# Kernel tuning notes

Measured on AMD Instinct MI355X. Metric: run time of the kernel, lower is better.

The kernel has to match this reference:

```python
import jax, jax.numpy as jnp
import numpy as np
from jax import lax

E = 16          # num_experts
CAP = 256       # capacity
MAX_IT = 3      # max_iterations
LPF = 2.0       # load_penalty_factor
DTEMP = 2.0     # diversity_temp
MIN_USAGE = 0.05
NC = 10         # num_classes
TC = 256        # trunk_channels
B = 2048
MIN_TOK = max(1, int(B * MIN_USAGE))        # 102
K_STATIC = min(B, max(CAP, MIN_TOK))        # static top-k width per expert claim


def setup_inputs() -> dict:
    key = jax.random.key(0)
    ks = jax.random.split(key, 16)
    d = {}
    d['x'] = jax.random.normal(ks[0], (B, 3, 32, 32), jnp.float32)
    chans = [(3, 32), (32, 64), (64, 128), (128, 256)]
    for i, (ci, co) in enumerate(chans, 1):
        d[f'cw{i}'] = jax.random.normal(ks[i], (co, ci, 3, 3), jnp.float32) * (1.0 / np.sqrt(ci * 9))
        d[f'cb{i}'] = jnp.zeros((co,), jnp.float32)
        d[f'g{i}'] = jnp.ones((co,), jnp.float32)
        d[f'be{i}'] = jnp.zeros((co,), jnp.float32)
        d[f'm{i}'] = jnp.zeros((co,), jnp.float32)
        d[f'v{i}'] = jnp.ones((co,), jnp.float32)
    d['gw1'] = jax.random.normal(ks[5], (E, TC, TC // 2), jnp.float32) * 0.05
    d['gb1'] = jnp.zeros((E, TC // 2), jnp.float32)
    d['gw2'] = jax.random.normal(ks[6], (E, TC // 2), jnp.float32) * 0.05
    d['gb2'] = jnp.zeros((E,), jnp.float32)
    d['cls_w'] = jax.random.normal(ks[7], (E, NC, TC), jnp.float32) * 0.01
    d['cls_b'] = jnp.zeros((E, NC), jnp.float32)
    d['usage_ema'] = jnp.ones((E,), jnp.float32) / E
    return d


def _conv_bn_relu(x, w, b, g, beta, m, v):
    y = lax.conv_general_dilated(x, w, (1, 1), 'SAME', dimension_numbers=('NCHW', 'OIHW', 'NCHW'))
    y = y + b[None, :, None, None]
    scale = (g / jnp.sqrt(v + 1e-5))[None, :, None, None]
    return jax.nn.relu((y - m[None, :, None, None]) * scale + beta[None, :, None, None])


def _maxpool2(x):
    return lax.reduce_window(x, -jnp.inf, lax.max, (1, 1, 2, 2), (1, 1, 2, 2), 'VALID')


def _forward(x, cw1, cb1, g1, be1, m1, v1, cw2, cb2, g2, be2, m2, v2,
             cw3, cb3, g3, be3, m3, v3, cw4, cb4, g4, be4, m4, v4,
             gw1, gb1, gw2, gb2, cls_w, cls_b, usage_ema):
    # trunk (eval-mode BN)
    h = _conv_bn_relu(x, cw1, cb1, g1, be1, m1, v1)
    h = _conv_bn_relu(h, cw2, cb2, g2, be2, m2, v2)
    h = _maxpool2(h)
    h = _conv_bn_relu(h, cw3, cb3, g3, be3, m3, v3)
    h = _conv_bn_relu(h, cw4, cb4, g4, be4, m4, v4)
    h = _maxpool2(h)
    feats = h.mean(axis=(2, 3))  # AdaptiveAvgPool2d(1)+Flatten -> [B, TC]

    # per-expert classifier heads
    logits_e = jnp.einsum('bd,ecd->bec', feats, cls_w) + cls_b[None]  # [B,E,NC]
    probs = jax.nn.softmax(logits_e, axis=2)
    ent = -(probs * jnp.log(jnp.clip(probs, 1e-12))).sum(axis=2)      # [B,E]
    confidence = -ent

    # per-expert gates (vectorized over experts); dropout is identity in eval
    hidden = jax.nn.relu(jnp.einsum('bd,edh->beh', feats, gw1) + gb1[None])
    expert_scores = (jnp.einsum('beh,eh->be', hidden, gw2) + gb2[None]) / DTEMP

    routing_scores = 0.6 * expert_scores + 0.4 * confidence - LPF * usage_ema[None]

    # iterative capacity-constrained routing (eval: expert order 0..E-1)
    D = jnp.zeros((B, E), bool)
    loads = jnp.zeros((E,), jnp.float32)
    avail = jnp.ones((B,), bool)
    ranks = jnp.arange(K_STATIC)
    for it in range(MAX_IT):
        # penalty from loads at the START of the iteration
        pscores = routing_scores - (it + 1) * LPF * loads[None]
        for j in range(E):
            sj = jnp.where(avail, pscores[:, j], -jnp.inf)
            vc = avail.sum().astype(jnp.int32)
            rc = jnp.maximum(0, CAP - loads[j].astype(jnp.int32))
            ntc = jnp.where((rc == 0) | (vc == 0), 0,
                            jnp.maximum(jnp.minimum(rc, vc), jnp.minimum(MIN_TOK, vc)))
            _, idx = lax.top_k(sj, K_STATIC)
            take = ranks < ntc
            claimed = jnp.zeros((B,), bool).at[idx].set(take)
            D = D.at[:, j].set(D[:, j] | claimed)
            avail = avail & ~claimed
            loads = loads.at[j].add(ntc.astype(jnp.float32))

    # fallback: sequentially assign leftover tokens to least-loaded of top-3
    def fb(carry, inp):
        Dc, lc = carry
        sc, av, i = inp
        _, t3 = lax.top_k(sc, 3)
        best = t3[jnp.argmin(lc[t3])]
        Dc = Dc.at[i, best].set(Dc[i, best] | av)
        lc = lc.at[best].add(av.astype(jnp.float32))
        return (Dc, lc), None

    (D, loads), _ = lax.scan(fb, (D, loads), (routing_scores, avail, jnp.arange(B)))

    Df = D.astype(jnp.float32)
    active = routing_scores * Df
    active = active - active.max(axis=1, keepdims=True)
    weights = jax.nn.softmax(active + (Df - 1.0) * 1e9, axis=1)
    final_logits = (weights[:, :, None] * logits_e).sum(axis=1)
    return final_logits, routing_scores, D


def reference(x, cw1, cb1, g1, be1, m1, v1, cw2, cb2, g2, be2, m2, v2,
              cw3, cb3, g3, be3, m3, v3, cw4, cb4, g4, be4, m4, v4,
              gw1, gb1, gw2, gb2, cls_w, cls_b, usage_ema):
    return _forward(x, cw1, cb1, g1, be1, m1, v1, cw2, cb2, g2, be2, m2, v2,
                    cw3, cb3, g3, be3, m3, v3, cw4, cb4, g4, be4, m4, v4,
                    gw1, gb1, gw2, gb2, cls_w, cls_b, usage_ema)
```

## Files before the change

kernel.cpp:

```cpp
#include <hip/hip_runtime.h>

typedef __attribute__((ext_vector_type(8))) short short8;
typedef __attribute__((ext_vector_type(4))) float f32x4;

__device__ __forceinline__ unsigned short f2bf(float f) {
  unsigned u = __float_as_uint(f);
  unsigned r = (u + 0x7fffu + ((u >> 16) & 1u)) >> 16;
  return (unsigned short)r;
}
__device__ __forceinline__ float bf2f(unsigned short h) {
  return __uint_as_float(((unsigned)h) << 16);
}

__global__ __launch_bounds__(256) void bnprep_kernel(
    const float* __restrict__ g, const float* __restrict__ be,
    const float* __restrict__ m, const float* __restrict__ v,
    const float* __restrict__ b, float* __restrict__ A, float* __restrict__ C, int n)
{
  int i = blockIdx.x * 256 + threadIdx.x;
  if (i < n) {
    float s = g[i] / sqrtf(v[i] + 1e-5f);
    A[i] = s;
    C[i] = (b[i] - m[i]) * s + be[i];
  }
}

__global__ __launch_bounds__(256) void wprep2_kernel(
    const float* __restrict__ w, unsigned short* __restrict__ wPk, int CO, int CI)
{
  int NCB = CI / 32, NF = CO / 16;
  int total = 9 * NCB * NF * 64;
  int idx = blockIdx.x * 256 + threadIdx.x;
  if (idx >= total) return;
  int lane = idx & 63;
  int unit = idx >> 6;
  int f = unit % NF;
  int cb = (unit / NF) % NCB;
  int s = unit / (NF * NCB);
  int co = f * 16 + (lane & 15);
  int ci0 = cb * 32 + (lane >> 4) * 8;
  long base = (long)unit * 1024 + lane * 8;
  #pragma unroll
  for (int j = 0; j < 8; ++j) {
    float v = w[((long)co * CI + ci0 + j) * 9 + s];
    unsigned short h = f2bf(v);
    unsigned short l = f2bf(v - bf2f(h));
    wPk[base + j] = h;
    wPk[base + 512 + j] = l;
  }
}

__global__ __launch_bounds__(512, 2) void conv12_kernel(
    const float* __restrict__ xin, const float* __restrict__ cw1,
    const float* __restrict__ A1p, const float* __restrict__ C1p,
    const unsigned short* __restrict__ wPk, const float* __restrict__ Ap,
    const float* __restrict__ Cp, unsigned short* __restrict__ outA)
{
  constexpr int TY = 16, TX = 32;
  constexpr int PXW = TX + 2;
  constexpr int PXT = (TY + 2) * PXW;
  constexpr int PLSTR = PXT * 8 + 8;
  constexpr int NF = 4;
  __shared__ alignas(16) unsigned short smem[8 * PLSTR];
  __shared__ alignas(16) float sx[2160];
  __shared__ alignas(16) float sw[864];

  const int nwg = gridDim.x;
  const int orig = blockIdx.x;
  const int q = nwg >> 3, r = nwg & 7;
  const int xcd = orig & 7, pos = orig >> 3;
  const int bx = (xcd < r ? xcd * (q + 1) : r * (q + 1) + (xcd - r) * q) + pos;

  const int img = bx >> 1;
  const int tY0 = (bx & 1) * 16;

  const int tid = threadIdx.x;
  const int lane = tid & 63;
  const int lx = lane & 15, kg = lane >> 4;
  const int w = tid >> 6;

  for (int i = tid; i < 2160; i += 512) {
    int c = i / 720, rem = i - c * 720;
    int yy = rem / 36, xx2 = rem - yy * 36;
    int gy = tY0 + yy - 2, gx = xx2 - 2;
    sx[i] = (gy >= 0 && gy < 32 && gx >= 0 && gx < 32)
            ? xin[(long)img * 3072 + c * 1024 + gy * 32 + gx] : 0.f;
  }
  for (int i = tid; i < 864; i += 512) {
    int co = i & 31, kk = i >> 5;
    sw[kk * 32 + co] = cw1[(long)co * 27 + kk];
  }
  __syncthreads();

  #pragma unroll 1
  for (int p = 0; p < 2; ++p) {
    int px = p * 512 + tid;
    if (px < PXT) {
      int ry = px / PXW, rx = px - ry * PXW;
      int gy = tY0 + ry - 1, gx = rx - 1;
      if (gy >= 0 && gy < 32 && gx >= 0 && gx < 32) {
        #pragma unroll 1
        for (int half = 0; half < 2; ++half) {
          float acc[16];
          #pragma unroll
          for (int j = 0; j < 16; ++j) acc[j] = 0.f;
          #pragma unroll
          for (int c = 0; c < 3; ++c) {
            #pragma unroll
            for (int k = 0; k < 9; ++k) {
              int dy = k / 3, dx = k - 3 * (k / 3);
              float iv = sx[c * 720 + (ry + dy) * 36 + rx + dx];
              const float4* w4 = (const float4*)(sw + (c * 9 + k) * 32 + half * 16);
              #pragma unroll
              for (int q2 = 0; q2 < 4; ++q2) {
                float4 wv = w4[q2];
                acc[4 * q2 + 0] += iv * wv.x; acc[4 * q2 + 1] += iv * wv.y;
                acc[4 * q2 + 2] += iv * wv.z; acc[4 * q2 + 3] += iv * wv.w;
              }
            }
          }
          #pragma unroll
          for (int j2 = 0; j2 < 2; ++j2) {
            short8 hv, lv;
            #pragma unroll
            for (int j = 0; j < 8; ++j) {
              int co = half * 16 + j2 * 8 + j;
              float vv = fmaxf(acc[j2 * 8 + j] * A1p[co] + C1p[co], 0.f);
              unsigned short h = f2bf(vv);
              hv[j] = (short)h;
              lv[j] = (short)f2bf(vv - bf2f(h));
            }
            int plane = half * 2 + j2;
            *(short8*)(smem + plane * PLSTR + px * 8) = hv;
            *(short8*)(smem + (plane + 4) * PLSTR + px * 8) = lv;
          }
        }
      } else {
        short8 zz = {0, 0, 0, 0, 0, 0, 0, 0};
        #pragma unroll
        for (int cc = 0; cc < 8; ++cc)
          *(short8*)(smem + cc * PLSTR + px * 8) = zz;
      }
    }
  }
  __syncthreads();

  f32x4 acc[4][4];
  #pragma unroll
  for (int i = 0; i < 4; ++i)
    #pragma unroll
    for (int j = 0; j < 4; ++j) acc[i][j] = (f32x4){0.f, 0.f, 0.f, 0.f};

  for (int s = 0; s < 9; ++s) {
    const int ky = s / 3, kx = s - 3 * (s / 3);
    const long ub = ((long)(s * NF)) * 1024 + lane * 8;
    short8 bh[4], bl[4];
    #pragma unroll
    for (int nf = 0; nf < 4; ++nf) {
      bh[nf] = *(const short8*)(wPk + ub + nf * 1024);
      bl[nf] = *(const short8*)(wPk + ub + nf * 1024 + 512);
    }
    #pragma unroll
    for (int mf = 0; mf < 4; ++mf) {
      const int yoff = mf >> 1;
      const int xb = (mf & 1) * 16;
      const int y = w * 2 + yoff;
      const int pxa = (y + ky) * PXW + xb + kx + lx;
      short8 ah = *(const short8*)(smem + kg * PLSTR + pxa * 8);
      short8 al = *(const short8*)(smem + (kg + 4) * PLSTR + pxa * 8);
      #pragma unroll
      for (int nf = 0; nf < 4; ++nf)
        acc[mf][nf] = __builtin_amdgcn_mfma_f32_16x16x32_bf16(ah, bh[nf], acc[mf][nf], 0, 0, 0);
      #pragma unroll
      for (int nf = 0; nf < 4; ++nf)
        acc[mf][nf] = __builtin_amdgcn_mfma_f32_16x16x32_bf16(ah, bl[nf], acc[mf][nf], 0, 0, 0);
      #pragma unroll
      for (int nf = 0; nf < 4; ++nf)
        acc[mf][nf] = __builtin_amdgcn_mfma_f32_16x16x32_bf16(al, bh[nf], acc[mf][nf], 0, 0, 0);
    }
  }
  __syncthreads();

  float Ar[4], Cr[4];
  #pragma unroll
  for (int nf = 0; nf < 4; ++nf) {
    int co = nf * 16 + lx;
    Ar[nf] = Ap[co]; Cr[nf] = Cp[co];
  }

  unsigned short* slice = smem + w * 2048;
  const int py = (tY0 >> 1) + w;
  #pragma unroll
  for (int xf = 0; xf < 2; ++xf) {
    #pragma unroll
    for (int rp = 0; rp < 2; ++rp) {
      int ox = xf * 8 + 2 * kg + rp;
      #pragma unroll
      for (int nf = 0; nf < 4; ++nf) {
        float v0 = fmaxf(fmaxf(acc[xf][nf][2 * rp], acc[xf][nf][2 * rp + 1]),
                         fmaxf(acc[xf + 2][nf][2 * rp], acc[xf + 2][nf][2 * rp + 1]));
        float vv = fmaxf(v0 * Ar[nf] + Cr[nf], 0.f);
        unsigned short h = f2bf(vv);
        unsigned short l = f2bf(vv - bf2f(h));
        slice[(ox * 2 + 0) * 64 + nf * 16 + lx] = h;
        slice[(ox * 2 + 1) * 64 + nf * 16 + lx] = l;
      }
    }
  }
  #pragma unroll
  for (int v = 0; v < 4; ++v) {
    int hoff = lane * 8 + v * 512;
    int x2 = hoff >> 7, rem = hoff & 127;
    int seg = rem >> 6, inner = rem & 63;
    short8 d = *(const short8*)(slice + hoff);
    *(short8*)(outA + ((long)img * 256 + py * 16 + x2) * 128 + seg * 64 + inner) = d;
  }
}

template<int H, int CI, int CO, int COB, int TY, int TX, int MODE>
__global__ __launch_bounds__(512, 2) void convmf4_kernel(
    const unsigned short* __restrict__ actIn, const unsigned short* __restrict__ wPk,
    const float* __restrict__ Ap, const float* __restrict__ Cp,
    void* __restrict__ outP)
{
  constexpr int NCB = CI / 32;
  constexpr int NF  = CO / 16;
  constexpr int NCOG = COB / 64;
  constexpr int NPXG = 8 / NCOG;
  constexpr int ROWS_PG = TY / NPXG;
  constexpr int FRX = TX / 16;
  constexpr int PXW = TX + 2;
  constexpr int PXT = (TY + 2) * PXW;
  constexpr int PLSTR = PXT * 8 + 8;
  constexpr int TILES_Y = H / TY;
  constexpr int CBLK = CO / COB;
  constexpr int TPI = TILES_Y * CBLK;
  constexpr int PIX_IN = 2 * CI;
  __shared__ alignas(16) unsigned short smem[8 * PLSTR];

  const int nwg = gridDim.x;
  const int orig = blockIdx.x;
  const int q = nwg >> 3, r = nwg & 7;
  const int xcd = orig & 7, pos = orig >> 3;
  const int bx = (xcd < r ? xcd * (q + 1) : r * (q + 1) + (xcd - r) * q) + pos;

  const int img = bx / TPI;
  const int sub = bx % TPI;
  const int tY0 = (sub % TILES_Y) * TY;
  const int blkco = sub / TILES_Y;

  const int tid = threadIdx.x;
  const int lane = tid & 63;
  const int lx = lane & 15, kg = lane >> 4;
  const int w = tid >> 6;
  const int pxg = w % NPXG, cog = w / NPXG;

  f32x4 acc[4][4];
  #pragma unroll
  for (int i = 0; i < 4; ++i)
    #pragma unroll
    for (int j = 0; j < 4; ++j) acc[i][j] = (f32x4){0.f, 0.f, 0.f, 0.f};

  for (int cb = 0; cb < NCB; ++cb) {
    if (cb) __syncthreads();
    for (int t2 = tid; t2 < PXT * 8; t2 += 512) {
      int px = t2 >> 3, c = t2 & 7;
      int ry = px / PXW, rx = px - ry * PXW;
      int gy = tY0 + ry - 1, gx = rx - 1;
      float4 v = (float4){0.f, 0.f, 0.f, 0.f};
      if (gy >= 0 && gy < H && gx >= 0 && gx < H) {
        int coff = (c < 4) ? (cb * 32 + c * 8) : (CI + cb * 32 + (c - 4) * 8);
        v = *(const float4*)(actIn + ((long)img * H * H + gy * H + gx) * PIX_IN + coff);
      }
      *(float4*)(smem + c * PLSTR + px * 8) = v;
    }
    __syncthreads();

    for (int s = 0; s < 9; ++s) {
      const int ky = s / 3, kx = s - 3 * (s / 3);
      const long ub = ((long)(s * NCB + cb) * NF + blkco * (COB / 16) + cog * 4) * 1024
                      + lane * 8;
      short8 bh[4], bl[4];
      #pragma unroll
      for (int nf = 0; nf < 4; ++nf) {
        bh[nf] = *(const short8*)(wPk + ub + nf * 1024);
        bl[nf] = *(const short8*)(wPk + ub + nf * 1024 + 512);
      }
      #pragma unroll
      for (int mf = 0; mf < 4; ++mf) {
        const int yoff = (FRX == 2) ? (mf >> 1) : mf;
        const int xb = (FRX == 2) ? ((mf & 1) * 16) : 0;
        const int y = pxg * ROWS_PG + yoff;
        const int pxa = (y + ky) * PXW + xb + kx + lx;
        short8 ah = *(const short8*)(smem + kg * PLSTR + pxa * 8);
        short8 al = *(const short8*)(smem + (kg + 4) * PLSTR + pxa * 8);
        #pragma unroll
        for (int nf = 0; nf < 4; ++nf)
          acc[mf][nf] = __builtin_amdgcn_mfma_f32_16x16x32_bf16(ah, bh[nf], acc[mf][nf], 0, 0, 0);
        #pragma unroll
        for (int nf = 0; nf < 4; ++nf)
          acc[mf][nf] = __builtin_amdgcn_mfma_f32_16x16x32_bf16(ah, bl[nf], acc[mf][nf], 0, 0, 0);
        #pragma unroll
        for (int nf = 0; nf < 4; ++nf)
          acc[mf][nf] = __builtin_amdgcn_mfma_f32_16x16x32_bf16(al, bh[nf], acc[mf][nf], 0, 0, 0);
      }
    }
  }
  __syncthreads();

  float Ar[4], Cr[4];
  #pragma unroll
  for (int nf = 0; nf < 4; ++nf) {
    int co = blkco * COB + cog * 64 + nf * 16 + lx;
    Ar[nf] = Ap[co]; Cr[nf] = Cp[co];
  }

  if (MODE == 0) {
    unsigned short* outA = (unsigned short*)outP;
    unsigned short* slice = smem + w * 2048;
    #pragma unroll
    for (int mf = 0; mf < 4; ++mf) {
      int y = tY0 + pxg * ROWS_PG + mf;
      #pragma unroll
      for (int rr = 0; rr < 4; ++rr) {
        int x = 4 * kg + rr;
        #pragma unroll
        for (int nf = 0; nf < 4; ++nf) {
          float vv = fmaxf(acc[mf][nf][rr] * Ar[nf] + Cr[nf], 0.f);
          unsigned short h = f2bf(vv);
          unsigned short l = f2bf(vv - bf2f(h));
          slice[(x * 2 + 0) * 64 + nf * 16 + lx] = h;
          slice[(x * 2 + 1) * 64 + nf * 16 + lx] = l;
        }
      }
      #pragma unroll
      for (int v = 0; v < 4; ++v) {
        int hoff = lane * 8 + v * 512;
        int x2 = hoff >> 7, rem = hoff & 127;
        int seg = rem >> 6, inner = rem & 63;
        short8 d = *(const short8*)(slice + hoff);
        *(short8*)(outA + ((long)img * 256 + y * 16 + x2) * (2 * CO)
                   + seg * CO + blkco * COB + cog * 64 + inner) = d;
      }
    }
  } else {
    float psum[4] = {0.f, 0.f, 0.f, 0.f};
    #pragma unroll
    for (int nf = 0; nf < 4; ++nf) {
      #pragma unroll
      for (int mfp = 0; mfp < 2; ++mfp) {
        #pragma unroll
        for (int rp = 0; rp < 2; ++rp) {
          float v = fmaxf(fmaxf(acc[2 * mfp][nf][2 * rp], acc[2 * mfp][nf][2 * rp + 1]),
                          fmaxf(acc[2 * mfp + 1][nf][2 * rp], acc[2 * mfp + 1][nf][2 * rp + 1]));
          psum[nf] += fmaxf(v * Ar[nf] + Cr[nf], 0.f);
        }
      }
    }
    #pragma unroll
    for (int nf = 0; nf < 4; ++nf) {
      psum[nf] += __shfl_xor(psum[nf], 16);
      psum[nf] += __shfl_xor(psum[nf], 32);
    }
    __syncthreads();
    float* sR = (float*)smem;
    if (kg == 0) {
      #pragma unroll
      for (int nf = 0; nf < 4; ++nf) sR[w * 64 + nf * 16 + lx] = psum[nf];
    }
    __syncthreads();
    if (tid < COB) {
      int ct = tid >> 6, ci_ = tid & 63;
      float s = 0.f;
      #pragma unroll
      for (int p = 0; p < NPXG; ++p) s += sR[(ct * NPXG + p) * 64 + ci_];
      ((float*)outP)[(long)img * 256 + blkco * COB + tid] = s * (1.f / 64.f);
    }
  }
}

__global__ __launch_bounds__(256) void heads2_kernel(
    const float* __restrict__ feats, const float* __restrict__ gw1,
    const float* __restrict__ gb1, const float* __restrict__ gw2,
    const float* __restrict__ gb2, const float* __restrict__ clsw,
    const float* __restrict__ clsb, const float* __restrict__ usage,
    float* __restrict__ logits_e, float* __restrict__ rs_out)
{
  __shared__ float sF[64 * 257];
  __shared__ float sLg[4 * 64 * 10];
  __shared__ float sRed[4 * 64];
  const int tid = threadIdx.x;
  const int b0 = blockIdx.x * 64;
  const int e  = blockIdx.y;

  for (int idx = tid; idx < 64 * 64; idx += 256) {
    int t = idx >> 6, dg = idx & 63;
    float4 v = ((const float4*)(feats + (long)(b0 + t) * 256))[dg];
    float* p = sF + t * 257 + dg * 4;
    p[0] = v.x; p[1] = v.y; p[2] = v.z; p[3] = v.w;
  }
  __syncthreads();

  const int t  = tid & 63;
  const int hw = __builtin_amdgcn_readfirstlane(tid >> 6);

  {
    float acc[10];
    #pragma unroll
    for (int c = 0; c < 10; ++c) acc[c] = 0.f;
    const float* fp = sF + t * 257 + hw * 64;
    const float* cw = clsw + (long)e * 2560 + hw * 64;
    for (int dd = 0; dd < 64; ++dd) {
      float f = fp[dd];
      #pragma unroll
      for (int c = 0; c < 10; ++c) acc[c] += f * cw[c * 256 + dd];
    }
    #pragma unroll
    for (int c = 0; c < 10; ++c) sLg[(hw * 64 + t) * 10 + c] = acc[c];
  }
  {
    float gacc[32];
    #pragma unroll
    for (int j = 0; j < 32; ++j) gacc[j] = 0.f;
    const float* wb = gw1 + ((long)e * 256) * 128 + hw * 32;
    const float* fp = sF + t * 257;
    for (int d = 0; d < 256; ++d) {
      float f = fp[d];
      const float4* w4 = (const float4*)(wb + (long)d * 128);
      #pragma unroll
      for (int qq = 0; qq < 8; ++qq) {
        float4 wv = w4[qq];
        gacc[4 * qq + 0] += f * wv.x; gacc[4 * qq + 1] += f * wv.y;
        gacc[4 * qq + 2] += f * wv.z; gacc[4 * qq + 3] += f * wv.w;
      }
    }
    float s = 0.f;
    const float* b1 = gb1 + e * 128 + hw * 32;
    const float* w2 = gw2 + e * 128 + hw * 32;
    #pragma unroll
    for (int j = 0; j < 32; ++j) s += fmaxf(gacc[j] + b1[j], 0.f) * w2[j];
    sRed[hw * 64 + t] = s;
  }
  __syncthreads();

  if (tid < 64) {
    float es = (sRed[t] + sRed[64 + t] + sRed[128 + t] + sRed[192 + t] + gb2[e]) * 0.5f;
    float lg[10];
    #pragma unroll
    for (int c = 0; c < 10; ++c)
      lg[c] = sLg[t * 10 + c] + sLg[(64 + t) * 10 + c]
            + sLg[(128 + t) * 10 + c] + sLg[(192 + t) * 10 + c] + clsb[e * 10 + c];
    float mx = lg[0];
    #pragma unroll
    for (int c = 1; c < 10; ++c) mx = fmaxf(mx, lg[c]);
    float S = 0.f, ps[10];
    #pragma unroll
    for (int c = 0; c < 10; ++c) { ps[c] = expf(lg[c] - mx); S += ps[c]; }
    float inv = 1.f / S, ent = 0.f;
    #pragma unroll
    for (int c = 0; c < 10; ++c) { float p = ps[c] * inv; ent -= p * logf(fmaxf(p, 1e-12f)); }
    float rsv = 0.6f * es + 0.4f * (-ent) - 2.0f * usage[e];
    rs_out[(long)(b0 + t) * 16 + e] = rsv;
    #pragma unroll
    for (int c = 0; c < 10; ++c)
      logits_e[((long)(b0 + t) * 16 + e) * 10 + c] = lg[c];
  }
}

__global__ __launch_bounds__(1024) void sort_kernel(
    const float* __restrict__ rs, unsigned* __restrict__ sortedIdx)
{
  __shared__ unsigned long long sk[2048];
  const int e = blockIdx.x;
  const unsigned tid = threadIdx.x;
  for (int i = tid; i < 2048; i += 1024) {
    float f = rs[(long)i * 16 + e];
    unsigned u = __float_as_uint(f);
    u ^= (u >> 31) ? 0xFFFFFFFFu : 0x80000000u;
    sk[i] = ((unsigned long long)(~u) << 32) | (unsigned)i;
  }
  for (unsigned k = 2; k <= 2048; k <<= 1) {
    for (unsigned j = k >> 1; j > 0; j >>= 1) {
      __syncthreads();
      unsigned i = ((tid & ~(j - 1)) << 1) | (tid & (j - 1));
      unsigned p = i | j;
      bool asc = ((i & k) == 0);
      unsigned long long a = sk[i], b = sk[p];
      if ((a > b) == asc) { sk[i] = b; sk[p] = a; }
    }
  }
  __syncthreads();
  for (int i = tid; i < 2048; i += 1024)
    sortedIdx[(long)e * 2048 + i] = (unsigned)(sk[i] & 0xFFFFFFFFull);
}

__global__ __launch_bounds__(1024) void routing_kernel(
    const unsigned* __restrict__ sortedIdx, const float* __restrict__ rs,
    float* __restrict__ Dout, unsigned* __restrict__ dmaskOut)
{
  __shared__ unsigned char sAvail[2048];
  __shared__ unsigned sDm[2048];
  __shared__ int sLoads[16];
  __shared__ int sWaveCnt[16];
  __shared__ int sNtc, sVC;
  const int tid = threadIdx.x;
  const int lane = tid & 63, wave = tid >> 6;
  for (int i = tid; i < 2048; i += 1024) { sAvail[i] = 1; sDm[i] = 0; }
  if (tid < 16) sLoads[tid] = 0;
  if (tid == 0) sVC = 2048;
  __syncthreads();
  for (int it = 0; it < 3; ++it) {
    for (int j = 0; j < 16; ++j) {
      if (tid == 0) {
        int rc = 256 - sLoads[j]; if (rc < 0) rc = 0;
        int vc = sVC, ntc = 0;
        if (rc > 0 && vc > 0) {
          int a = rc < vc ? rc : vc;
          int b2 = vc < 102 ? vc : 102;
          ntc = a > b2 ? a : b2;
        }
        sNtc = ntc; sLoads[j] += ntc; sVC -= ntc;
      }
      __syncthreads();
      const int ntc = sNtc;
      if (ntc > 0) {
        int base = 0;
        for (int p = 0; p < 2; ++p) {
          int i = p * 1024 + tid;
          unsigned tok = sortedIdx[(long)j * 2048 + i];
          int fl = sAvail[tok] ? 1 : 0;
          unsigned long long bm = __ballot(fl);
          if (lane == 0) sWaveCnt[wave] = __popcll(bm);
          __syncthreads();
          int off = base;
          for (int w = 0; w < wave; ++w) off += sWaveCnt[w];
          int pre = off + __popcll(bm & ((1ull << lane) - 1ull));
          if (fl && pre < ntc) { sAvail[tok] = 0; sDm[tok] |= (1u << j); }
          int tot = base;
          for (int w = 0; w < 16; ++w) tot += sWaveCnt[w];
          base = tot;
          __syncthreads();
        }
      }
      __syncthreads();
    }
  }
  if (tid == 0 && sVC > 0) {
    for (int i = 0; i < 2048; ++i) {
      if (!sAvail[i]) continue;
      float s0 = -3.4e38f, s1 = s0, s2 = s0; int e0 = 0, e1 = 0, e2 = 0;
      for (int e = 0; e < 16; ++e) {
        float s = rs[i * 16 + e];
        if (s > s0)      { s2 = s1; e2 = e1; s1 = s0; e1 = e0; s0 = s; e0 = e; }
        else if (s > s1) { s2 = s1; e2 = e1; s1 = s;  e1 = e; }
        else if (s > s2) { s2 = s;  e2 = e; }
      }
      int best = e0, bl = sLoads[e0];
      if (sLoads[e1] < bl) { best = e1; bl = sLoads[e1]; }
      if (sLoads[e2] < bl) { best = e2; bl = sLoads[e2]; }
      sDm[i] |= (1u << best);
      sLoads[best] += 1;
    }
  }
  __syncthreads();
  for (int idx = tid; idx < 2048 * 16; idx += 1024) {
    int tok = idx >> 4, e = idx & 15;
    Dout[idx] = ((sDm[tok] >> e) & 1u) ? 1.0f : 0.0f;
  }
  for (int i = tid; i < 2048; i += 1024) dmaskOut[i] = sDm[i];
}

__global__ __launch_bounds__(256) void combine_kernel(
    const unsigned* __restrict__ dmask, const float* __restrict__ rs,
    const float* __restrict__ L, float* __restrict__ out)
{
  int i = blockIdx.x * 256 + threadIdx.x;
  if (i >= 2048) return;
  unsigned dm = dmask[i];
  float r[16];
  #pragma unroll
  for (int e = 0; e < 16; ++e) r[e] = rs[i * 16 + e];
  float mx = -3.4e38f;
  #pragma unroll
  for (int e = 0; e < 16; ++e) {
    float v = ((dm >> e) & 1u) ? r[e] : 0.0f;
    mx = fmaxf(mx, v);
  }
  float w[16], S = 0.f;
  #pragma unroll
  for (int e = 0; e < 16; ++e) {
    w[e] = ((dm >> e) & 1u) ? expf(r[e] - mx) : 0.0f;
    S += w[e];
  }
  float inv = 1.f / S;
  #pragma unroll
  for (int c = 0; c < 10; ++c) {
    float a = 0.f;
    #pragma unroll
    for (int e = 0; e < 16; ++e) a += w[e] * L[((long)i * 16 + e) * 10 + c];
    out[i * 10 + c] = a * inv;
  }
}

extern "C" void kernel_launch(void* const* d_in, const int* in_sizes, int n_in,
                              void* d_out, int out_size, void* d_ws, size_t ws_size,
                              hipStream_t stream)
{
  const float* x    = (const float*)d_in[0];
  const float* cw1  = (const float*)d_in[1];
  const float* cb1  = (const float*)d_in[2];
  const float* g1   = (const float*)d_in[3];
  const float* be1  = (const float*)d_in[4];
  const float* m1   = (const float*)d_in[5];
  const float* v1   = (const float*)d_in[6];
  const float* cw2  = (const float*)d_in[7];
  const float* cb2  = (const float*)d_in[8];
  const float* g2   = (const float*)d_in[9];
  const float* be2  = (const float*)d_in[10];
  const float* m2   = (const float*)d_in[11];
  const float* v2   = (const float*)d_in[12];
  const float* cw3  = (const float*)d_in[13];
  const float* cb3  = (const float*)d_in[14];
  const float* g3   = (const float*)d_in[15];
  const float* be3  = (const float*)d_in[16];
  const float* m3   = (const float*)d_in[17];
  const float* v3   = (const float*)d_in[18];
  const float* cw4  = (const float*)d_in[19];
  const float* cb4  = (const float*)d_in[20];
  const float* g4   = (const float*)d_in[21];
  const float* be4  = (const float*)d_in[22];
  const float* m4   = (const float*)d_in[23];
  const float* v4   = (const float*)d_in[24];
  const float* gw1  = (const float*)d_in[25];
  const float* gb1  = (const float*)d_in[26];
  const float* gw2  = (const float*)d_in[27];
  const float* gb2  = (const float*)d_in[28];
  const float* clsw = (const float*)d_in[29];
  const float* clsb = (const float*)d_in[30];
  const float* usage = (const float*)d_in[31];

  float* out = (float*)d_out;
  float* ws  = (float*)d_ws;

  float* A1 = ws + 0;   float* C1 = ws + 32;
  float* A2 = ws + 64;  float* C2 = ws + 128;
  float* A3 = ws + 192; float* C3 = ws + 320;
  float* A4 = ws + 448; float* C4 = ws + 704;
  float* feats   = ws + 1024;
  float* logitsE = ws + 525312;
  unsigned* sortedIdx = (unsigned*)(ws + 852992);
  unsigned* dmask     = (unsigned*)(ws + 885760);
  unsigned short* wPk2 = (unsigned short*)(ws + 887808);
  unsigned short* wPk3 = (unsigned short*)(ws + 906240);
  unsigned short* wPk4 = (unsigned short*)(ws + 979968);
  const long bufBase = 1274880;

  long wsFloats = (long)(ws_size / 4);
  long availF = wsFloats - bufBase;
  long chunkL = availF / 49152;
  int chunk = (int)(chunkL < 1 ? 1 : (chunkL > 2048 ? 2048 : chunkL));

  bnprep_kernel<<<1, 256, 0, stream>>>(g1, be1, m1, v1, cb1, A1, C1, 32);
  bnprep_kernel<<<1, 256, 0, stream>>>(g2, be2, m2, v2, cb2, A2, C2, 64);
  bnprep_kernel<<<1, 256, 0, stream>>>(g3, be3, m3, v3, cb3, A3, C3, 128);
  bnprep_kernel<<<1, 256, 0, stream>>>(g4, be4, m4, v4, cb4, A4, C4, 256);
  wprep2_kernel<<<(2304 + 255) / 256, 256, 0, stream>>>(cw2, wPk2, 64, 32);
  wprep2_kernel<<<(9216 + 255) / 256, 256, 0, stream>>>(cw3, wPk3, 128, 64);
  wprep2_kernel<<<(36864 + 255) / 256, 256, 0, stream>>>(cw4, wPk4, 256, 128);

  unsigned short* bufA = (unsigned short*)(ws + bufBase);
  unsigned short* bufB = bufA + (long)chunk * 65536;

  for (int ib = 0; ib < 2048; ib += chunk) {
    int n = 2048 - ib; if (n > chunk) n = chunk;
    conv12_kernel<<<dim3(n * 2), 512, 0, stream>>>(
        x + (long)ib * 3072, cw1, A1, C1, wPk2, A2, C2, bufB);
    convmf4_kernel<16, 64, 128, 128, 16, 16, 0>
        <<<dim3(n), 512, 0, stream>>>(bufB, wPk3, A3, C3, bufA);
    convmf4_kernel<16, 128, 256, 128, 16, 16, 2>
        <<<dim3(n * 2), 512, 0, stream>>>(bufA, wPk4, A4, C4, feats + (long)ib * 256);
  }

  float* rsOut = out + 20480;
  heads2_kernel<<<dim3(32, 16), 256, 0, stream>>>(feats, gw1, gb1, gw2, gb2,
                                                  clsw, clsb, usage, logitsE, rsOut);
  sort_kernel<<<16, 1024, 0, stream>>>(rsOut, sortedIdx);
  routing_kernel<<<1, 1024, 0, stream>>>(sortedIdx, rsOut, out + 53248, dmask);
  combine_kernel<<<8, 256, 0, stream>>>(dmask, rsOut, logitsE, out);
}
```

Before: 1.417 ms.

## Run greedy routing in a single wavefront with early exit, move D write to combine

```diff
diff --git a/kernel.cpp b/kernel.cpp
--- a/kernel.cpp
+++ b/kernel.cpp
@@ -494,85 +494,76 @@
     sortedIdx[(long)e * 2048 + i] = (unsigned)(sk[i] & 0xFFFFFFFFull);
 }
 
-__global__ __launch_bounds__(1024) void routing_kernel(
+__global__ __launch_bounds__(64) void routing2_kernel(
     const unsigned* __restrict__ sortedIdx, const float* __restrict__ rs,
-    float* __restrict__ Dout, unsigned* __restrict__ dmaskOut)
+    unsigned* __restrict__ dmaskOut)
 {
   __shared__ unsigned char sAvail[2048];
   __shared__ unsigned sDm[2048];
   __shared__ int sLoads[16];
-  __shared__ int sWaveCnt[16];
-  __shared__ int sNtc, sVC;
-  const int tid = threadIdx.x;
-  const int lane = tid & 63, wave = tid >> 6;
-  for (int i = tid; i < 2048; i += 1024) { sAvail[i] = 1; sDm[i] = 0; }
-  if (tid < 16) sLoads[tid] = 0;
-  if (tid == 0) sVC = 2048;
-  __syncthreads();
+  const int lane = threadIdx.x;
+  for (int i = lane; i < 2048; i += 64) { sAvail[i] = 1; sDm[i] = 0; }
+  if (lane < 16) sLoads[lane] = 0;
+  __syncthreads();
+
+  int vc = 2048;
   for (int it = 0; it < 3; ++it) {
     for (int j = 0; j < 16; ++j) {
-      if (tid == 0) {
-        int rc = 256 - sLoads[j]; if (rc < 0) rc = 0;
-        int vc = sVC, ntc = 0;
-        if (rc > 0 && vc > 0) {
-          int a = rc < vc ? rc : vc;
-          int b2 = vc < 102 ? vc : 102;
-          ntc = a > b2 ? a : b2;
-        }
-        sNtc = ntc; sLoads[j] += ntc; sVC -= ntc;
-      }
-      __syncthreads();
-      const int ntc = sNtc;
+      int lj = sLoads[j];
+      int rc = 256 - lj; if (rc < 0) rc = 0;
+      int ntc = 0;
+      if (rc > 0 && vc > 0) {
+        int a = rc < vc ? rc : vc;
+        int b2 = vc < 102 ? vc : 102;
+        ntc = a > b2 ? a : b2;
+      }
       if (ntc > 0) {
-        int base = 0;
-        for (int p = 0; p < 2; ++p) {
-          int i = p * 1024 + tid;
-          unsigned tok = sortedIdx[(long)j * 2048 + i];
+        const unsigned* se = sortedIdx + (long)j * 2048;
+        int taken = 0;
+        for (int base = 0; base < 2048; base += 64) {
+          if (taken >= ntc) break;
+          unsigned tok = se[base + lane];
           int fl = sAvail[tok] ? 1 : 0;
           unsigned long long bm = __ballot(fl);
-          if (lane == 0) sWaveCnt[wave] = __popcll(bm);
-          __syncthreads();
-          int off = base;
-          for (int w = 0; w < wave; ++w) off += sWaveCnt[w];
-          int pre = off + __popcll(bm & ((1ull << lane) - 1ull));
+          int pre = taken + __popcll(bm & ((1ull << lane) - 1ull));
           if (fl && pre < ntc) { sAvail[tok] = 0; sDm[tok] |= (1u << j); }
-          int tot = base;
-          for (int w = 0; w < 16; ++w) tot += sWaveCnt[w];
-          base = tot;
+          taken += (int)__popcll(bm);
           __syncthreads();
         }
-      }
-      __syncthreads();
-    }
-  }
-  if (tid == 0 && sVC > 0) {
-    for (int i = 0; i < 2048; ++i) {
-      if (!sAvail[i]) continue;
-      float s0 = -3.4e38f, s1 = s0, s2 = s0; int e0 = 0, e1 = 0, e2 = 0;
-      for (int e = 0; e < 16; ++e) {
-        float s = rs[i * 16 + e];
-        if (s > s0)      { s2 = s1; e2 = e1; s1 = s0; e1 = e0; s0 = s; e0 = e; }
-        else if (s > s1) { s2 = s1; e2 = e1; s1 = s;  e1 = e; }
-        else if (s > s2) { s2 = s;  e2 = e; }
-      }
-      int best = e0, bl = sLoads[e0];
-      if (sLoads[e1] < bl) { best = e1; bl = sLoads[e1]; }
-      if (sLoads[e2] < bl) { best = e2; bl = sLoads[e2]; }
-      sDm[i] |= (1u << best);
-      sLoads[best] += 1;
-    }
-  }
-  __syncthreads();
-  for (int idx = tid; idx < 2048 * 16; idx += 1024) {
-    int tok = idx >> 4, e = idx & 15;
-    Dout[idx] = ((sDm[tok] >> e) & 1u) ? 1.0f : 0.0f;
-  }
-  for (int i = tid; i < 2048; i += 1024) dmaskOut[i] = sDm[i];
+        if (lane == 0) sLoads[j] = lj + ntc;
+        vc -= ntc;
+        __syncthreads();
+      }
+    }
+  }
+
+  if (vc > 0) {
+    if (lane == 0) {
+      for (int i = 0; i < 2048; ++i) {
+        if (!sAvail[i]) continue;
+        float s0 = -3.4e38f, s1 = s0, s2 = s0; int e0 = 0, e1 = 0, e2 = 0;
+        for (int e = 0; e < 16; ++e) {
+          float s = rs[i * 16 + e];
+          if (s > s0)      { s2 = s1; e2 = e1; s1 = s0; e1 = e0; s0 = s; e0 = e; }
+          else if (s > s1) { s2 = s1; e2 = e1; s1 = s;  e1 = e; }
+          else if (s > s2) { s2 = s;  e2 = e; }
+        }
+        int best = e0, bl = sLoads[e0];
+        if (sLoads[e1] < bl) { best = e1; bl = sLoads[e1]; }
+        if (sLoads[e2] < bl) { best = e2; bl = sLoads[e2]; }
+        sDm[i] |= (1u << best);
+        sLoads[best] += 1;
+      }
+    }
+    __syncthreads();
+  }
+
+  for (int i = lane; i < 2048; i += 64) dmaskOut[i] = sDm[i];
 }
 
 __global__ __launch_bounds__(256) void combine_kernel(
     const unsigned* __restrict__ dmask, const float* __restrict__ rs,
-    const float* __restrict__ L, float* __restrict__ out)
+    const float* __restrict__ L, float* __restrict__ out, float* __restrict__ Dout)
 {
   int i = blockIdx.x * 256 + threadIdx.x;
   if (i >= 2048) return;
@@ -600,6 +591,9 @@
     for (int e = 0; e < 16; ++e) a += w[e] * L[((long)i * 16 + e) * 10 + c];
     out[i * 10 + c] = a * inv;
   }
+  #pragma unroll
+  for (int e = 0; e < 16; ++e)
+    Dout[(long)i * 16 + e] = ((dm >> e) & 1u) ? 1.0f : 0.0f;
 }
 
 extern "C" void kernel_launch(void* const* d_in, const int* in_sizes, int n_in,
@@ -685,6 +679,6 @@
   heads2_kernel<<<dim3(32, 16), 256, 0, stream>>>(feats, gw1, gb1, gw2, gb2,
                                                   clsw, clsb, usage, logitsE, rsOut);
   sort_kernel<<<16, 1024, 0, stream>>>(rsOut, sortedIdx);
-  routing_kernel<<<1, 1024, 0, stream>>>(sortedIdx, rsOut, out + 53248, dmask);
-  combine_kernel<<<8, 256, 0, stream>>>(dmask, rsOut, logitsE, out);
-}
+  routing2_kernel<<<1, 64, 0, stream>>>(sortedIdx, rsOut, dmask);
+  combine_kernel<<<8, 256, 0, stream>>>(dmask, rsOut, logitsE, out, out + 53248);
+}
```

Measured after the change: 1.420 ms. About the same (+0.2%).
